# Kernel optimization log

Hardware: AMD Instinct MI355X
Metric: run time of the kernel (lower is better)

## Reference

```python
import jax, jax.numpy as jnp
import numpy as np

N, E, NF, EF = 50000, 1600000, 16, 8
H, HEADS, HD, L = 128, 4, 32, 3
EPS = 1e-5
NEG_SLOPE = 0.2


def layer_norm(x, g, b):
    mu = jnp.mean(x, axis=-1, keepdims=True)
    var = jnp.mean((x - mu) ** 2, axis=-1, keepdims=True)
    return g * (x - mu) * jax.lax.rsqrt(var + EPS) + b


def setup_inputs() -> dict:
    key = jax.random.key(0)
    ks = jax.random.split(key, 16)
    s = 0.02
    return {
        "x": jax.random.normal(ks[0], (N, NF), jnp.float32),
        "edge_index": jax.random.randint(ks[1], (2, E), 0, N, jnp.int32),
        "edge_attr": jax.random.normal(ks[2], (E, EF), jnp.float32),
        "Wn": jax.random.normal(ks[3], (NF, H), jnp.float32) * s,
        "bn": jnp.zeros((H,), jnp.float32),
        "We": jax.random.normal(ks[4], (EF, H), jnp.float32) * s,
        "be": jnp.zeros((H,), jnp.float32),
        "ln_g": jnp.ones((L, H), jnp.float32),
        "ln_b": jnp.zeros((L, H), jnp.float32),
        "Wg": jax.random.normal(ks[5], (L, H, HEADS * HD), jnp.float32) * s,
        "att_s": jax.random.normal(ks[6], (L, HEADS, HD), jnp.float32) * s,
        "att_d": jax.random.normal(ks[7], (L, HEADS, HD), jnp.float32) * s,
        "att_e": jax.random.normal(ks[8], (L, HEADS, HD), jnp.float32) * s,
        "W_edge": jax.random.normal(ks[9], (L, H, HEADS * HD), jnp.float32) * s,
        "bg": jnp.zeros((L, HEADS * HD), jnp.float32),
    }


def reference(x, edge_index, edge_attr, Wn, bn, We, be, ln_g, ln_b, Wg, att_s, att_d, att_e, W_edge, bg):
    n = x.shape[0]
    h = x @ Wn + bn                      # [N, H] node embedding
    e = edge_attr @ We + be              # [E, H] edge embedding
    src, dst = edge_index[0], edge_index[1]
    # PyG add_self_loops(fill_value='mean'): self-loop attr = mean of incoming edge attrs
    cnt = jax.ops.segment_sum(jnp.ones((e.shape[0],), e.dtype), dst, num_segments=n)
    loop_attr = jax.ops.segment_sum(e, dst, num_segments=n) / jnp.maximum(cnt, 1.0)[:, None]
    ar = jnp.arange(n, dtype=src.dtype)
    src_f = jnp.concatenate([src, ar])   # [E+N]
    dst_f = jnp.concatenate([dst, ar])
    e_f = jnp.concatenate([e, loop_attr], axis=0)  # [E+N, H]
    for i in range(Wg.shape[0]):
        x_in = layer_norm(h, ln_g[i], ln_b[i])               # pre-norm
        xs = (x_in @ Wg[i]).reshape(n, HEADS, HD)            # [N, heads, hd]
        ep = (e_f @ W_edge[i]).reshape(-1, HEADS, HD)        # [E+N, heads, hd]
        a_src = jnp.sum(xs * att_s[i], axis=-1)              # [N, heads]
        a_dst = jnp.sum(xs * att_d[i], axis=-1)
        a_edge = jnp.sum(ep * att_e[i], axis=-1)             # [E+N, heads]
        alpha = jax.nn.leaky_relu(a_src[src_f] + a_dst[dst_f] + a_edge, NEG_SLOPE)
        # scatter-softmax over edges sharing a destination node
        alpha = alpha - jax.ops.segment_max(alpha, dst_f, num_segments=n)[dst_f]
        ex = jnp.exp(alpha)
        w = ex / jax.ops.segment_sum(ex, dst_f, num_segments=n)[dst_f]  # [E+N, heads]
        msg = w[:, :, None] * xs[src_f]                      # [E+N, heads, hd]
        out = jax.ops.segment_sum(msg, dst_f, num_segments=n).reshape(n, HEADS * HD) + bg[i]
        h = h + jax.nn.relu(out)                             # proj is Identity; dropout eval-mode
    graph_emb = jnp.mean(h, axis=0, keepdims=True)           # batch=None path
    return h, graph_emb
```

## Files before the change

### kernel.cpp

```cpp
#include <hip/hip_runtime.h>

#define NN 50000
#define EE 1600000
#define HC 128
#define EPSV 1e-5f
#define NEGS 0.2f

#define NB_H0 6250
#define NB_HIST 6250
#define NB_PREP 230

typedef __bf16 bf16x8 __attribute__((ext_vector_type(8)));
typedef __bf16 bf16x2 __attribute__((ext_vector_type(2)));
typedef float f32x4 __attribute__((ext_vector_type(4)));

static inline int cdiv(int a, int b) { return (a + b - 1) / b; }

__device__ inline float blo(unsigned v) { return __uint_as_float(v << 16); }
__device__ inline float bhi(unsigned v) { return __uint_as_float(v & 0xffff0000u); }
__device__ inline unsigned pkbf(float a, float b) {
  bf16x2 p;
  p.x = (__bf16)a;
  p.y = (__bf16)b;
  return *reinterpret_cast<unsigned*>(&p);
}

__device__ inline float dec_e4m3(unsigned u) {
  unsigned bits = ((u & 0x80u) << 24) | ((u & 0x7Fu) << 20);
  return __uint_as_float(bits) * 0x1p120f;
}
__device__ inline unsigned enc_e4m3(float v) {
  unsigned b = __float_as_uint(v * 0x1p-120f);
  unsigned mag = (b & 0x7fffffffu) + 0x00080000u;
  return ((b >> 24) & 0x80u) | ((mag >> 20) & 0x7Fu);
}
__device__ inline unsigned enc4_e4m3(const float* r) {
  return enc_e4m3(r[0]) | (enc_e4m3(r[1]) << 8) | (enc_e4m3(r[2]) << 16) | (enc_e4m3(r[3]) << 24);
}

__global__ __launch_bounds__(256) void k_pre(const float* __restrict__ x, const float* __restrict__ Wn,
                                             const float* __restrict__ bn, const float* __restrict__ lng,
                                             const float* __restrict__ lnb, float* __restrict__ h,
                                             __bf16* __restrict__ xln, const int* __restrict__ ei,
                                             int* __restrict__ cnt, const float* __restrict__ We,
                                             const float* __restrict__ be, const float* __restrict__ Wed,
                                             const float* __restrict__ atte, float* __restrict__ Pc,
                                             const float* __restrict__ Wg, const float* __restrict__ atts,
                                             const float* __restrict__ attd, __bf16* __restrict__ wgt,
                                             int nb_hist) {
  int b = blockIdx.x;
  int t = threadIdx.x;
  if (b < NB_H0) {
    int idx = b * 256 + t;
    int n = idx >> 5, c4 = (idx & 31) * 4;
    float4 acc = *(const float4*)(bn + c4);
    const float* xr = x + (size_t)n * 16;
#pragma unroll
    for (int f = 0; f < 16; ++f) {
      float xv = xr[f];
      float4 wv = *(const float4*)(Wn + (size_t)f * HC + c4);
      acc.x += xv * wv.x;
      acc.y += xv * wv.y;
      acc.z += xv * wv.z;
      acc.w += xv * wv.w;
    }
    *(float4*)(h + (size_t)n * HC + c4) = acc;
    float s = acc.x + acc.y + acc.z + acc.w;
    float sq = acc.x * acc.x + acc.y * acc.y + acc.z * acc.z + acc.w * acc.w;
#pragma unroll
    for (int m = 1; m < 32; m <<= 1) {
      s += __shfl_xor(s, m);
      sq += __shfl_xor(sq, m);
    }
    float mu = s * (1.f / 128.f);
    float var = sq * (1.f / 128.f) - mu * mu;
    float rs = rsqrtf(fmaxf(var, 0.f) + EPSV);
    float4 g = *(const float4*)(lng + c4);
    float4 bb = *(const float4*)(lnb + c4);
    uint2 o;
    o.x = pkbf((acc.x - mu) * rs * g.x + bb.x, (acc.y - mu) * rs * g.y + bb.y);
    o.y = pkbf((acc.z - mu) * rs * g.z + bb.z, (acc.w - mu) * rs * g.w + bb.w);
    *(uint2*)(xln + (size_t)n * HC + c4) = o;
  } else if (b < NB_H0 + nb_hist) {
    int e = (b - NB_H0) * 256 + t;
    if (e < EE) atomicAdd(&cnt[ei[EE + e]], 1);
  } else if (b == NB_H0 + nb_hist) {
    __shared__ float v[128][4];
    for (int i = 0; i < 3; ++i) {
      if (t < 128) {
#pragma unroll
        for (int hh = 0; hh < 4; ++hh) {
          float s = 0.f;
          for (int hd = 0; hd < 32; ++hd)
            s += Wed[((size_t)i * 128 + t) * 128 + hh * 32 + hd] * atte[i * 128 + hh * 32 + hd];
          v[t][hh] = s;
        }
      }
      __syncthreads();
      if (t < 32) {
        int f = t >> 2, hh = t & 3;
        float s = 0.f;
        for (int c2 = 0; c2 < 128; ++c2) s += We[f * 128 + c2] * v[c2][hh];
        Pc[i * 36 + f * 4 + hh] = s;
      }
      if (t < 4) {
        float s = 0.f;
        for (int c2 = 0; c2 < 128; ++c2) s += be[c2] * v[c2][t];
        Pc[i * 36 + 32 + t] = s;
      }
      __syncthreads();
    }
  } else {
    int idx = (b - NB_H0 - nb_hist - 1) * 256 + t;
    if (idx >= 3 * 144 * 136) return;
    int i = idx / (144 * 136);
    int rem = idx - i * (144 * 136);
    int n = rem / 136, kp = rem - n * 136;
    float v = 0.f;
    if (kp < 128) {
      if (n < 128) {
        v = Wg[(size_t)i * 16384 + kp * 128 + n];
      } else if (n < 136) {
        int hh = (n - 128) & 3;
        const float* av = ((n < 132) ? atts : attd) + i * 128 + hh * 32;
        const float* wr = Wg + (size_t)i * 16384 + kp * 128 + hh * 32;
        float s = 0.f;
#pragma unroll
        for (int j = 0; j < 32; ++j) s += wr[j] * av[j];
        v = s;
      }
    }
    wgt[idx] = (__bf16)v;
  }
}

__global__ __launch_bounds__(1024) void k_scan1(const int* __restrict__ cnt, int* __restrict__ tmp,
                                                int* __restrict__ bsum) {
  __shared__ int lds[1024];
  int t = threadIdx.x;
  int i = blockIdx.x * 1024 + t;
  int v = (i < NN) ? cnt[i] : 0;
  lds[t] = v;
  __syncthreads();
  for (int off = 1; off < 1024; off <<= 1) {
    int u = (t >= off) ? lds[t - off] : 0;
    __syncthreads();
    lds[t] += u;
    __syncthreads();
  }
  if (i < NN) tmp[i] = lds[t] - v;
  if (t == 1023) bsum[blockIdx.x] = lds[1023];
}

__global__ void k_scan2(int* bsum, int nb) {
  if (threadIdx.x == 0 && blockIdx.x == 0) {
    int run = 0;
    for (int b = 0; b < nb; ++b) { int q = bsum[b]; bsum[b] = run; run += q; }
  }
}

__global__ __launch_bounds__(1024) void k_scan3(const int* __restrict__ tmp, const int* __restrict__ bsum,
                                                int* __restrict__ row_ptr, int* __restrict__ wr_ptr) {
  int t = threadIdx.x;
  int i = blockIdx.x * 1024 + t;
  if (i < NN) {
    int v = tmp[i] + bsum[blockIdx.x];
    row_ptr[i] = v;
    wr_ptr[i] = v;
  }
  if (i == 0) row_ptr[NN] = EE;
}

__global__ __launch_bounds__(256) void k_build(const int* __restrict__ ei, const float* __restrict__ ea,
                                               const float* __restrict__ Pc, int* __restrict__ cntr,
                                               unsigned char* __restrict__ rec8, int cap) {
  __shared__ float P[108];
  if (threadIdx.x < 108) P[threadIdx.x] = Pc[threadIdx.x];
  __syncthreads();
  int e = blockIdx.x * 256 + threadIdx.x;
  if (e >= EE) return;
  int s = ei[e], d = ei[EE + e];
  const float* ar = ea + (size_t)e * 8;
  float4 q0 = *(const float4*)ar;
  float4 q1 = *(const float4*)(ar + 4);
  float a[8] = {q0.x, q0.y, q0.z, q0.w, q1.x, q1.y, q1.z, q1.w};
  float r[3][4];
#pragma unroll
  for (int i = 0; i < 3; ++i) {
    const float* p = P + i * 36;
#pragma unroll
    for (int hh = 0; hh < 4; ++hh) {
      float s2 = p[32 + hh];
#pragma unroll
      for (int f = 0; f < 8; ++f) s2 += a[f] * p[f * 4 + hh];
      r[i][hh] = s2;
    }
  }
  size_t idx;
  int pos = atomicAdd(&cntr[d], 1);
  if (cap == 0) {
    idx = (size_t)pos;
  } else {
    if (pos >= cap) return;
    idx = (size_t)d * cap + pos;
  }
  uint4 rr;
  rr.x = (unsigned)s;
  rr.y = enc4_e4m3(r[0]);
  rr.z = enc4_e4m3(r[1]);
  rr.w = enc4_e4m3(r[2]);
  *(uint4*)(rec8 + idx * 16) = rr;
}

__global__ __launch_bounds__(256) void k_node(const __bf16* __restrict__ xln, const __bf16* __restrict__ wgt,
                                              __bf16* __restrict__ xsb, float* __restrict__ asrc,
                                              float* __restrict__ adst) {
  __shared__ __bf16 sA[128][136];
  __shared__ __bf16 sB[144][136];
  int t = threadIdx.x;
  int n0 = blockIdx.x * 128;
  {
    char* bd = (char*)&sB[0][0];
    const char* bs = (const char*)wgt;
    for (int off = t * 16; off < 144 * 136 * 2; off += 4096)
      *(uint4*)(bd + off) = *(const uint4*)(bs + off);
  }
  {
    uint4 z = make_uint4(0, 0, 0, 0);
#pragma unroll
    for (int u = t; u < 128 * 16; u += 256) {
      int row = u >> 4, ck = (u & 15) * 8;
      int n = n0 + row;
      uint4 v = (n < NN) ? *(const uint4*)(xln + (size_t)n * HC + ck) : z;
      *(uint4*)&sA[row][ck] = v;
    }
  }
  __syncthreads();
  int lane = t & 63;
  int c15 = lane & 15, g = lane >> 4;
  int m0w = (t >> 6) * 32;
  f32x4 acc[18];
#pragma unroll
  for (int i = 0; i < 18; ++i) acc[i] = (f32x4){0.f, 0.f, 0.f, 0.f};
#pragma unroll
  for (int ks = 0; ks < 4; ++ks) {
    bf16x8 a0 = *(const bf16x8*)&sA[m0w + c15][ks * 32 + g * 8];
    bf16x8 a1 = *(const bf16x8*)&sA[m0w + 16 + c15][ks * 32 + g * 8];
#pragma unroll
    for (int nt = 0; nt < 9; ++nt) {
      bf16x8 bv = *(const bf16x8*)&sB[nt * 16 + c15][ks * 32 + g * 8];
      acc[nt] = __builtin_amdgcn_mfma_f32_16x16x32_bf16(a0, bv, acc[nt], 0, 0, 0);
      acc[9 + nt] = __builtin_amdgcn_mfma_f32_16x16x32_bf16(a1, bv, acc[9 + nt], 0, 0, 0);
    }
  }
#pragma unroll
  for (int mt = 0; mt < 2; ++mt) {
    int nbase = n0 + m0w + mt * 16 + g * 4;
#pragma unroll
    for (int r = 0; r < 4; ++r) {
      int n = nbase + r;
      if (n < NN) {
        __bf16* op = xsb + (size_t)n * HC + c15;
#pragma unroll
        for (int nt = 0; nt < 8; ++nt) op[nt * 16] = (__bf16)acc[mt * 9 + nt][r];
        float av = acc[mt * 9 + 8][r];
        if (c15 < 4) asrc[(size_t)n * 4 + c15] = av;
        else if (c15 < 8) adst[(size_t)n * 4 + c15 - 4] = av;
      }
    }
  }
}

__global__ __launch_bounds__(256) void k_aggr(const int* __restrict__ row_ptr, const int* __restrict__ deg,
                                              int cap, const unsigned char* __restrict__ rec8, int layer,
                                              const __bf16* __restrict__ xsb, const float* __restrict__ asrc,
                                              const float* __restrict__ adst, const float* __restrict__ bgi,
                                              float* __restrict__ h, const float* __restrict__ lng2,
                                              const float* __restrict__ lnb2, __bf16* __restrict__ xln) {
  int wid = (blockIdx.x * 256 + threadIdx.x) >> 6;
  if (wid >= NN) return;
  int lane = threadIdx.x & 63;
  int ch0 = 2 * lane, head = lane >> 4;
  int um = lane & 7;
  int sbase = head << 4;
  int aoff = 4 + 4 * layer + head;
  int j0, j1;
  if (cap == 0) {
    j0 = row_ptr[wid];
    j1 = row_ptr[wid + 1];
  } else {
    j0 = wid * cap;
    int dg = deg[wid];
    if (dg > cap) dg = cap;
    j1 = j0 + dg;
  }
  float ad = adst[(size_t)wid * 4 + head];
  float acc0 = 0.f, acc1 = 0.f, dsum = 0.f, aes = 0.f;
  int nfull = (j1 - j0) >> 3;
  int j = j0 + nfull * 8;
  if (nfull > 0) {
    int ss[8], ssn[8];
#pragma unroll
    for (int u = 0; u < 8; ++u) ss[u] = *(const int*)(rec8 + (size_t)(j0 + u) * 16);
    for (int c = 0; c < nfull; ++c) {
      int jc = j0 + c * 8;
      if (c + 1 < nfull) {
#pragma unroll
        for (int u = 0; u < 8; ++u) ssn[u] = *(const int*)(rec8 + (size_t)(jc + 8 + u) * 16);
      } else {
#pragma unroll
        for (int u = 0; u < 8; ++u) ssn[u] = ss[u];
      }
      float av = dec_e4m3(rec8[(size_t)(jc + um) * 16 + aoff]);
      float as = asrc[(size_t)ss[um] * 4 + head];
      unsigned xv[8];
#pragma unroll
      for (int u = 0; u < 8; ++u) xv[u] = *(const unsigned*)(xsb + (size_t)ss[u] * HC + ch0);
      float alpha = as + ad + av;
      alpha = alpha > 0.f ? alpha : NEGS * alpha;
      float em = __expf(alpha);
      aes += av;
#pragma unroll
      for (int u = 0; u < 8; ++u) {
        float e = __shfl(em, sbase + u);
        acc0 += e * blo(xv[u]);
        acc1 += e * bhi(xv[u]);
        dsum += e;
      }
#pragma unroll
      for (int u = 0; u < 8; ++u) ss[u] = ssn[u];
    }
  }
  aes += __shfl_xor(aes, 1);
  aes += __shfl_xor(aes, 2);
  aes += __shfl_xor(aes, 4);
  for (; j < j1; ++j) {
    int s0 = *(const int*)(rec8 + (size_t)j * 16);
    float v0 = dec_e4m3(rec8[(size_t)j * 16 + aoff]);
    float as0 = asrc[(size_t)s0 * 4 + head];
    unsigned x0 = *(const unsigned*)(xsb + (size_t)s0 * HC + ch0);
    float a0 = as0 + ad + v0;
    a0 = a0 > 0.f ? a0 : NEGS * a0;
    float e0 = __expf(a0);
    acc0 += e0 * blo(x0);
    acc1 += e0 * bhi(x0);
    dsum += e0;
    aes += v0;
  }
  int dg = j1 - j0;
  float aself = (dg > 0) ? aes / (float)dg : 0.f;
  float al = asrc[(size_t)wid * 4 + head] + ad + aself;
  al = al > 0.f ? al : NEGS * al;
  float exl = __expf(al);
  unsigned xv = *(const unsigned*)(xsb + (size_t)wid * HC + ch0);
  float inv = 1.f / (dsum + exl);
  float o0 = (acc0 + exl * blo(xv)) * inv;
  float o1 = (acc1 + exl * bhi(xv)) * inv;
  float* hp = h + (size_t)wid * HC;
  float n0v = hp[ch0] + fmaxf(0.f, o0 + bgi[ch0]);
  float n1v = hp[ch0 + 1] + fmaxf(0.f, o1 + bgi[ch0 + 1]);
  hp[ch0] = n0v;
  hp[ch0 + 1] = n1v;
  if (xln) {
    float s = n0v + n1v, sq = n0v * n0v + n1v * n1v;
#pragma unroll
    for (int m = 1; m < 64; m <<= 1) {
      s += __shfl_xor(s, m);
      sq += __shfl_xor(sq, m);
    }
    float mu = s * (1.f / 128.f);
    float var = sq * (1.f / 128.f) - mu * mu;
    float rs = rsqrtf(fmaxf(var, 0.f) + EPSV);
    unsigned p = pkbf((n0v - mu) * rs * lng2[ch0] + lnb2[ch0], (n1v - mu) * rs * lng2[ch0 + 1] + lnb2[ch0 + 1]);
    *(unsigned*)(xln + (size_t)wid * HC + ch0) = p;
  }
}

__global__ __launch_bounds__(256) void k_emb(const float* __restrict__ h, float* __restrict__ emb) {
  int t = blockIdx.x * 256 + threadIdx.x;
  int stride = gridDim.x * 256;
  float s = 0.f;
  for (int i = t; i < NN * HC; i += stride) s += h[i];
  __shared__ float red[256];
  red[threadIdx.x] = s;
  __syncthreads();
  if (threadIdx.x < 128) {
    float v2 = red[threadIdx.x] + red[threadIdx.x + 128];
    atomicAdd(&emb[threadIdx.x], v2 * (1.f / NN));
  }
}

extern "C" void kernel_launch(void* const* d_in, const int* in_sizes, int n_in, void* d_out, int out_size,
                              void* d_ws, size_t ws_size, hipStream_t stream) {
  (void)in_sizes; (void)n_in; (void)out_size;
  const float* x = (const float*)d_in[0];
  const int* ei = (const int*)d_in[1];
  const float* ea = (const float*)d_in[2];
  const float* Wn = (const float*)d_in[3];
  const float* bn = (const float*)d_in[4];
  const float* We = (const float*)d_in[5];
  const float* be = (const float*)d_in[6];
  const float* lng = (const float*)d_in[7];
  const float* lnb = (const float*)d_in[8];
  const float* Wg = (const float*)d_in[9];
  const float* atts = (const float*)d_in[10];
  const float* attd = (const float*)d_in[11];
  const float* atte = (const float*)d_in[12];
  const float* Wed = (const float*)d_in[13];
  const float* bg = (const float*)d_in[14];
  float* h = (float*)d_out;
  float* emb = h + (size_t)NN * HC;

  char* w = (char*)d_ws;
  size_t off = 0;
  auto alloc = [&](size_t bytes) {
    void* p = w + off;
    off = (off + bytes + 255) & ~(size_t)255;
    return p;
  };
  __bf16* xsb = (__bf16*)alloc((size_t)NN * HC * 2);
  __bf16* xln = (__bf16*)alloc((size_t)NN * HC * 2);
  float* asrc = (float*)alloc((size_t)NN * 4 * 4);
  float* adst = (float*)alloc((size_t)NN * 4 * 4);
  int* cnt = (int*)alloc((size_t)NN * 4);
  int* row_ptr = (int*)alloc((size_t)(NN + 1) * 4);
  int* wr_ptr = (int*)alloc((size_t)NN * 4);
  int* bsum = (int*)alloc(256);
  int* stmp = (int*)alloc((size_t)NN * 4);
  float* Pc = (float*)alloc(3 * 36 * 4);
  __bf16* wgt = (__bf16*)alloc((size_t)3 * 144 * 136 * 2);

  size_t avail = (ws_size > off + 4096) ? (ws_size - off - 4096) : 0;
  size_t capv = avail / ((size_t)NN * 16);
  int cap = 0;
  if (capv >= 72) cap = (capv > 96) ? 96 : (int)capv;
  unsigned char* rec8 = (unsigned char*)alloc(cap ? (size_t)NN * cap * 16 : (size_t)EE * 16);

  hipMemsetAsync(cnt, 0, (size_t)NN * 4, stream);
  hipMemsetAsync(emb, 0, HC * 4, stream);

  if (cap) {
    k_pre<<<NB_H0 + 1 + NB_PREP, 256, 0, stream>>>(x, Wn, bn, lng, lnb, h, xln, ei, cnt, We, be, Wed, atte,
                                                   Pc, Wg, atts, attd, wgt, 0);
    k_build<<<cdiv(EE, 256), 256, 0, stream>>>(ei, ea, Pc, cnt, rec8, cap);
  } else {
    k_pre<<<NB_H0 + NB_HIST + 1 + NB_PREP, 256, 0, stream>>>(x, Wn, bn, lng, lnb, h, xln, ei, cnt, We, be,
                                                             Wed, atte, Pc, Wg, atts, attd, wgt, NB_HIST);
    int nb = cdiv(NN, 1024);
    k_scan1<<<nb, 1024, 0, stream>>>(cnt, stmp, bsum);
    k_scan2<<<1, 64, 0, stream>>>(bsum, nb);
    k_scan3<<<nb, 1024, 0, stream>>>(stmp, bsum, row_ptr, wr_ptr);
    k_build<<<cdiv(EE, 256), 256, 0, stream>>>(ei, ea, Pc, wr_ptr, rec8, 0);
  }

  for (int i = 0; i < 3; ++i) {
    k_node<<<cdiv(NN, 128), 256, 0, stream>>>(xln, wgt + (size_t)i * 144 * 136, xsb, asrc, adst);
    const float* g2 = (i < 2) ? (lng + (i + 1) * HC) : nullptr;
    const float* b2 = (i < 2) ? (lnb + (i + 1) * HC) : nullptr;
    __bf16* xo = (i < 2) ? xln : nullptr;
    k_aggr<<<cdiv(NN, 4), 256, 0, stream>>>(row_ptr, cnt, cap, rec8, i, xsb, asrc, adst, bg + i * HC, h,
                                            g2, b2, xo);
  }
  k_emb<<<512, 256, 0, stream>>>(h, emb);
}
```

Baseline: 420.7 us.

## Store node features as fp8 e4m3 and fuse layer-0 node GEMM into build

Changes the projected node feature buffer xs from bf16 to fp8 e4m3, which halves the bytes gathered per edge in the aggregation kernel at the cost of extra decode ALU work and lower precision. The layer-0 node GEMM is also merged into the edge-build launch as extra blocks, so it overlaps with the atomic-heavy build and one launch is saved. In the fallback path build and node are launched separately.

```diff
diff --git a/kernel.cpp b/kernel.cpp
--- a/kernel.cpp
+++ b/kernel.cpp
@@ -9,6 +9,8 @@
 #define NB_H0 6250
 #define NB_HIST 6250
 #define NB_PREP 230
+#define NB_BUILD 6250
+#define NB_NODE 391
 
 typedef __bf16 bf16x8 __attribute__((ext_vector_type(8)));
 typedef __bf16 bf16x2 __attribute__((ext_vector_type(2)));
@@ -171,13 +173,12 @@
   if (i == 0) row_ptr[NN] = EE;
 }
 
-__global__ __launch_bounds__(256) void k_build(const int* __restrict__ ei, const float* __restrict__ ea,
-                                               const float* __restrict__ Pc, int* __restrict__ cntr,
-                                               unsigned char* __restrict__ rec8, int cap) {
-  __shared__ float P[108];
-  if (threadIdx.x < 108) P[threadIdx.x] = Pc[threadIdx.x];
+__device__ inline void build_body(int bb, int t, const int* __restrict__ ei, const float* __restrict__ ea,
+                                  const float* __restrict__ Pc, int* __restrict__ cntr,
+                                  unsigned char* __restrict__ rec8, int cap, float* P) {
+  if (t < 108) P[t] = Pc[t];
   __syncthreads();
-  int e = blockIdx.x * 256 + threadIdx.x;
+  int e = bb * 256 + t;
   if (e >= EE) return;
   int s = ei[e], d = ei[EE + e];
   const float* ar = ea + (size_t)e * 8;
@@ -212,13 +213,10 @@
   *(uint4*)(rec8 + idx * 16) = rr;
 }
 
-__global__ __launch_bounds__(256) void k_node(const __bf16* __restrict__ xln, const __bf16* __restrict__ wgt,
-                                              __bf16* __restrict__ xsb, float* __restrict__ asrc,
-                                              float* __restrict__ adst) {
-  __shared__ __bf16 sA[128][136];
-  __shared__ __bf16 sB[144][136];
-  int t = threadIdx.x;
-  int n0 = blockIdx.x * 128;
+__device__ inline void node_body(int nb, int t, const __bf16* __restrict__ xln, const __bf16* __restrict__ wgt,
+                                 unsigned char* __restrict__ xsb, float* __restrict__ asrc,
+                                 float* __restrict__ adst, __bf16 (*sA)[136], __bf16 (*sB)[136]) {
+  int n0 = nb * 128;
   {
     char* bd = (char*)&sB[0][0];
     const char* bs = (const char*)wgt;
@@ -260,9 +258,9 @@
     for (int r = 0; r < 4; ++r) {
       int n = nbase + r;
       if (n < NN) {
-        __bf16* op = xsb + (size_t)n * HC + c15;
-#pragma unroll
-        for (int nt = 0; nt < 8; ++nt) op[nt * 16] = (__bf16)acc[mt * 9 + nt][r];
+        unsigned char* op = xsb + (size_t)n * HC + c15;
+#pragma unroll
+        for (int nt = 0; nt < 8; ++nt) op[nt * 16] = (unsigned char)enc_e4m3(acc[mt * 9 + nt][r]);
         float av = acc[mt * 9 + 8][r];
         if (c15 < 4) asrc[(size_t)n * 4 + c15] = av;
         else if (c15 < 8) adst[(size_t)n * 4 + c15 - 4] = av;
@@ -271,12 +269,38 @@
   }
 }
 
+__global__ __launch_bounds__(256) void k_bn(const int* __restrict__ ei, const float* __restrict__ ea,
+                                            const float* __restrict__ Pc, int* __restrict__ cntr,
+                                            unsigned char* __restrict__ rec8, int cap,
+                                            const __bf16* __restrict__ xln, const __bf16* __restrict__ wgt,
+                                            unsigned char* __restrict__ xsb, float* __restrict__ asrc,
+                                            float* __restrict__ adst, int nbuild) {
+  __shared__ __bf16 sA[128][136];
+  __shared__ __bf16 sB[144][136];
+  int b = blockIdx.x;
+  int t = threadIdx.x;
+  if (b < nbuild) {
+    build_body(b, t, ei, ea, Pc, cntr, rec8, cap, (float*)&sA[0][0]);
+  } else {
+    node_body(b - nbuild, t, xln, wgt, xsb, asrc, adst, sA, sB);
+  }
+}
+
+__global__ __launch_bounds__(256) void k_node(const __bf16* __restrict__ xln, const __bf16* __restrict__ wgt,
+                                              unsigned char* __restrict__ xsb, float* __restrict__ asrc,
+                                              float* __restrict__ adst) {
+  __shared__ __bf16 sA[128][136];
+  __shared__ __bf16 sB[144][136];
+  node_body(blockIdx.x, threadIdx.x, xln, wgt, xsb, asrc, adst, sA, sB);
+}
+
 __global__ __launch_bounds__(256) void k_aggr(const int* __restrict__ row_ptr, const int* __restrict__ deg,
                                               int cap, const unsigned char* __restrict__ rec8, int layer,
-                                              const __bf16* __restrict__ xsb, const float* __restrict__ asrc,
-                                              const float* __restrict__ adst, const float* __restrict__ bgi,
-                                              float* __restrict__ h, const float* __restrict__ lng2,
-                                              const float* __restrict__ lnb2, __bf16* __restrict__ xln) {
+                                              const unsigned char* __restrict__ xsb,
+                                              const float* __restrict__ asrc, const float* __restrict__ adst,
+                                              const float* __restrict__ bgi, float* __restrict__ h,
+                                              const float* __restrict__ lng2, const float* __restrict__ lnb2,
+                                              __bf16* __restrict__ xln) {
   int wid = (blockIdx.x * 256 + threadIdx.x) >> 6;
   if (wid >= NN) return;
   int lane = threadIdx.x & 63;
@@ -313,9 +337,10 @@
       }
       float av = dec_e4m3(rec8[(size_t)(jc + um) * 16 + aoff]);
       float as = asrc[(size_t)ss[um] * 4 + head];
-      unsigned xv[8];
-#pragma unroll
-      for (int u = 0; u < 8; ++u) xv[u] = *(const unsigned*)(xsb + (size_t)ss[u] * HC + ch0);
+      unsigned short xv[8];
+#pragma unroll
+      for (int u = 0; u < 8; ++u)
+        xv[u] = *(const unsigned short*)(xsb + (size_t)ss[u] * HC + ch0);
       float alpha = as + ad + av;
       alpha = alpha > 0.f ? alpha : NEGS * alpha;
       float em = __expf(alpha);
@@ -323,8 +348,8 @@
 #pragma unroll
       for (int u = 0; u < 8; ++u) {
         float e = __shfl(em, sbase + u);
-        acc0 += e * blo(xv[u]);
-        acc1 += e * bhi(xv[u]);
+        acc0 += e * dec_e4m3(xv[u] & 0xFFu);
+        acc1 += e * dec_e4m3((unsigned)xv[u] >> 8);
         dsum += e;
       }
 #pragma unroll
@@ -338,12 +363,12 @@
     int s0 = *(const int*)(rec8 + (size_t)j * 16);
     float v0 = dec_e4m3(rec8[(size_t)j * 16 + aoff]);
     float as0 = asrc[(size_t)s0 * 4 + head];
-    unsigned x0 = *(const unsigned*)(xsb + (size_t)s0 * HC + ch0);
+    unsigned short x0 = *(const unsigned short*)(xsb + (size_t)s0 * HC + ch0);
     float a0 = as0 + ad + v0;
     a0 = a0 > 0.f ? a0 : NEGS * a0;
     float e0 = __expf(a0);
-    acc0 += e0 * blo(x0);
-    acc1 += e0 * bhi(x0);
+    acc0 += e0 * dec_e4m3(x0 & 0xFFu);
+    acc1 += e0 * dec_e4m3((unsigned)x0 >> 8);
     dsum += e0;
     aes += v0;
   }
@@ -352,10 +377,10 @@
   float al = asrc[(size_t)wid * 4 + head] + ad + aself;
   al = al > 0.f ? al : NEGS * al;
   float exl = __expf(al);
-  unsigned xv = *(const unsigned*)(xsb + (size_t)wid * HC + ch0);
+  unsigned short xw = *(const unsigned short*)(xsb + (size_t)wid * HC + ch0);
   float inv = 1.f / (dsum + exl);
-  float o0 = (acc0 + exl * blo(xv)) * inv;
-  float o1 = (acc1 + exl * bhi(xv)) * inv;
+  float o0 = (acc0 + exl * dec_e4m3(xw & 0xFFu)) * inv;
+  float o1 = (acc1 + exl * dec_e4m3((unsigned)xw >> 8)) * inv;
   float* hp = h + (size_t)wid * HC;
   float n0v = hp[ch0] + fmaxf(0.f, o0 + bgi[ch0]);
   float n1v = hp[ch0 + 1] + fmaxf(0.f, o1 + bgi[ch0 + 1]);
@@ -418,7 +443,7 @@
     off = (off + bytes + 255) & ~(size_t)255;
     return p;
   };
-  __bf16* xsb = (__bf16*)alloc((size_t)NN * HC * 2);
+  unsigned char* xsb = (unsigned char*)alloc((size_t)NN * HC);
   __bf16* xln = (__bf16*)alloc((size_t)NN * HC * 2);
   float* asrc = (float*)alloc((size_t)NN * 4 * 4);
   float* adst = (float*)alloc((size_t)NN * 4 * 4);
@@ -442,7 +467,8 @@
   if (cap) {
     k_pre<<<NB_H0 + 1 + NB_PREP, 256, 0, stream>>>(x, Wn, bn, lng, lnb, h, xln, ei, cnt, We, be, Wed, atte,
                                                    Pc, Wg, atts, attd, wgt, 0);
-    k_build<<<cdiv(EE, 256), 256, 0, stream>>>(ei, ea, Pc, cnt, rec8, cap);
+    k_bn<<<NB_BUILD + NB_NODE, 256, 0, stream>>>(ei, ea, Pc, cnt, rec8, cap, xln, wgt, xsb, asrc, adst,
+                                                 NB_BUILD);
   } else {
     k_pre<<<NB_H0 + NB_HIST + 1 + NB_PREP, 256, 0, stream>>>(x, Wn, bn, lng, lnb, h, xln, ei, cnt, We, be,
                                                              Wed, atte, Pc, Wg, atts, attd, wgt, NB_HIST);
@@ -450,11 +476,13 @@
     k_scan1<<<nb, 1024, 0, stream>>>(cnt, stmp, bsum);
     k_scan2<<<1, 64, 0, stream>>>(bsum, nb);
     k_scan3<<<nb, 1024, 0, stream>>>(stmp, bsum, row_ptr, wr_ptr);
-    k_build<<<cdiv(EE, 256), 256, 0, stream>>>(ei, ea, Pc, wr_ptr, rec8, 0);
+    k_bn<<<cdiv(EE, 256), 256, 0, stream>>>(ei, ea, Pc, wr_ptr, rec8, 0, xln, wgt, xsb, asrc, adst,
+                                            cdiv(EE, 256));
+    k_node<<<NB_NODE, 256, 0, stream>>>(xln, wgt, xsb, asrc, adst);
   }
 
   for (int i = 0; i < 3; ++i) {
-    k_node<<<cdiv(NN, 128), 256, 0, stream>>>(xln, wgt + (size_t)i * 144 * 136, xsb, asrc, adst);
+    if (i > 0) k_node<<<NB_NODE, 256, 0, stream>>>(xln, wgt + (size_t)i * 144 * 136, xsb, asrc, adst);
     const float* g2 = (i < 2) ? (lng + (i + 1) * HC) : nullptr;
     const float* b2 = (i < 2) ? (lnb + (i + 1) * HC) : nullptr;
     __bf16* xo = (i < 2) ? xln : nullptr;
```

New measurement: 441.1 us. +4.8%, slower.

## Merge edge build with node init into one kernel; nontemporal edge record loads

Applied to the files above, without the earlier changes.

Moves the tiny edge-coefficient reduction into its own single-block kernel, then fuses the edge-record build, the initial node embedding and layer-norm, and the weight prep into one launch on the capped-bucket path. This drops a kernel boundary and lets the build blocks overlap with the node work. Edge record reads in the aggregation loop now use nontemporal loads so the streamed records do not evict reused node features from cache. The cost is an extra tiny serial kernel that runs ahead of the fused launch.

```diff
diff --git a/kernel.cpp b/kernel.cpp
--- a/kernel.cpp
+++ b/kernel.cpp
@@ -9,6 +9,8 @@
 #define NB_H0 6250
 #define NB_HIST 6250
 #define NB_PREP 230
+#define NB_BUILD 6250
+#define NB_NODE 391
 
 typedef __bf16 bf16x8 __attribute__((ext_vector_type(8)));
 typedef __bf16 bf16x2 __attribute__((ext_vector_type(2)));
@@ -38,100 +40,177 @@
   return enc_e4m3(r[0]) | (enc_e4m3(r[1]) << 8) | (enc_e4m3(r[2]) << 16) | (enc_e4m3(r[3]) << 24);
 }
 
-__global__ __launch_bounds__(256) void k_pre(const float* __restrict__ x, const float* __restrict__ Wn,
-                                             const float* __restrict__ bn, const float* __restrict__ lng,
-                                             const float* __restrict__ lnb, float* __restrict__ h,
-                                             __bf16* __restrict__ xln, const int* __restrict__ ei,
-                                             int* __restrict__ cnt, const float* __restrict__ We,
-                                             const float* __restrict__ be, const float* __restrict__ Wed,
-                                             const float* __restrict__ atte, float* __restrict__ Pc,
-                                             const float* __restrict__ Wg, const float* __restrict__ atts,
-                                             const float* __restrict__ attd, __bf16* __restrict__ wgt,
-                                             int nb_hist) {
-  int b = blockIdx.x;
+__global__ __launch_bounds__(128) void k_wcoef(const float* __restrict__ We, const float* __restrict__ be,
+                                               const float* __restrict__ Wed, const float* __restrict__ atte,
+                                               float* __restrict__ Pc) {
+  __shared__ float v[128][4];
   int t = threadIdx.x;
+  for (int i = 0; i < 3; ++i) {
+#pragma unroll
+    for (int hh = 0; hh < 4; ++hh) {
+      float s = 0.f;
+      for (int hd = 0; hd < 32; ++hd)
+        s += Wed[((size_t)i * 128 + t) * 128 + hh * 32 + hd] * atte[i * 128 + hh * 32 + hd];
+      v[t][hh] = s;
+    }
+    __syncthreads();
+    if (t < 32) {
+      int f = t >> 2, hh = t & 3;
+      float s = 0.f;
+      for (int c2 = 0; c2 < 128; ++c2) s += We[f * 128 + c2] * v[c2][hh];
+      Pc[i * 36 + f * 4 + hh] = s;
+    }
+    if (t < 4) {
+      float s = 0.f;
+      for (int c2 = 0; c2 < 128; ++c2) s += be[c2] * v[c2][t];
+      Pc[i * 36 + 32 + t] = s;
+    }
+    __syncthreads();
+  }
+}
+
+
+__device__ inline void h0_body(int idx, const float* __restrict__ x, const float* __restrict__ Wn,
+                               const float* __restrict__ bn, const float* __restrict__ lng,
+                               const float* __restrict__ lnb, float* __restrict__ h,
+                               __bf16* __restrict__ xln) {
+  int n = idx >> 5, c4 = (idx & 31) * 4;
+  float4 acc = *(const float4*)(bn + c4);
+  const float* xr = x + (size_t)n * 16;
+#pragma unroll
+  for (int f = 0; f < 16; ++f) {
+    float xv = xr[f];
+    float4 wv = *(const float4*)(Wn + (size_t)f * HC + c4);
+    acc.x += xv * wv.x;
+    acc.y += xv * wv.y;
+    acc.z += xv * wv.z;
+    acc.w += xv * wv.w;
+  }
+  *(float4*)(h + (size_t)n * HC + c4) = acc;
+  float s = acc.x + acc.y + acc.z + acc.w;
+  float sq = acc.x * acc.x + acc.y * acc.y + acc.z * acc.z + acc.w * acc.w;
+#pragma unroll
+  for (int m = 1; m < 32; m <<= 1) {
+    s += __shfl_xor(s, m);
+    sq += __shfl_xor(sq, m);
+  }
+  float mu = s * (1.f / 128.f);
+  float var = sq * (1.f / 128.f) - mu * mu;
+  float rs = rsqrtf(fmaxf(var, 0.f) + EPSV);
+  float4 g = *(const float4*)(lng + c4);
+  float4 bb = *(const float4*)(lnb + c4);
+  uint2 o;
+  o.x = pkbf((acc.x - mu) * rs * g.x + bb.x, (acc.y - mu) * rs * g.y + bb.y);
+  o.y = pkbf((acc.z - mu) * rs * g.z + bb.z, (acc.w - mu) * rs * g.w + bb.w);
+  *(uint2*)(xln + (size_t)n * HC + c4) = o;
+}
+
+__device__ inline void prep_body(int idx, const float* __restrict__ Wg, const float* __restrict__ atts,
+                                 const float* __restrict__ attd, __bf16* __restrict__ wgt) {
+  if (idx >= 3 * 144 * 136) return;
+  int i = idx / (144 * 136);
+  int rem = idx - i * (144 * 136);
+  int n = rem / 136, kp = rem - n * 136;
+  float v = 0.f;
+  if (kp < 128) {
+    if (n < 128) {
+      v = Wg[(size_t)i * 16384 + kp * 128 + n];
+    } else if (n < 136) {
+      int hh = (n - 128) & 3;
+      const float* av = ((n < 132) ? atts : attd) + i * 128 + hh * 32;
+      const float* wr = Wg + (size_t)i * 16384 + kp * 128 + hh * 32;
+      float s = 0.f;
+#pragma unroll
+      for (int j = 0; j < 32; ++j) s += wr[j] * av[j];
+      v = s;
+    }
+  }
+  wgt[idx] = (__bf16)v;
+}
+
+__device__ inline void build_body(int bb, int t, const int* __restrict__ ei, const float* __restrict__ ea,
+                                  const float* __restrict__ Pc, int* __restrict__ cntr,
+                                  unsigned char* __restrict__ rec8, int cap, float* P) {
+  if (t < 108) P[t] = Pc[t];
+  __syncthreads();
+  int e = bb * 256 + t;
+  if (e >= EE) return;
+  int s = ei[e], d = ei[EE + e];
+  const float* ar = ea + (size_t)e * 8;
+  float4 q0 = *(const float4*)ar;
+  float4 q1 = *(const float4*)(ar + 4);
+  float a[8] = {q0.x, q0.y, q0.z, q0.w, q1.x, q1.y, q1.z, q1.w};
+  float r[3][4];
+#pragma unroll
+  for (int i = 0; i < 3; ++i) {
+    const float* p = P + i * 36;
+#pragma unroll
+    for (int hh = 0; hh < 4; ++hh) {
+      float s2 = p[32 + hh];
+#pragma unroll
+      for (int f = 0; f < 8; ++f) s2 += a[f] * p[f * 4 + hh];
+      r[i][hh] = s2;
+    }
+  }
+  size_t idx;
+  int pos = atomicAdd(&cntr[d], 1);
+  if (cap == 0) {
+    idx = (size_t)pos;
+  } else {
+    if (pos >= cap) return;
+    idx = (size_t)d * cap + pos;
+  }
+  uint4 rr;
+  rr.x = (unsigned)s;
+  rr.y = enc4_e4m3(r[0]);
+  rr.z = enc4_e4m3(r[1]);
+  rr.w = enc4_e4m3(r[2]);
+  *(uint4*)(rec8 + idx * 16) = rr;
+}
+
+__global__ __launch_bounds__(256) void k_mega(const int* __restrict__ ei, const float* __restrict__ ea,
+                                              const float* __restrict__ Pc, int* __restrict__ cnt,
+                                              unsigned char* __restrict__ rec8, int cap,
+                                              const float* __restrict__ x, const float* __restrict__ Wn,
+                                              const float* __restrict__ bn, const float* __restrict__ lng,
+                                              const float* __restrict__ lnb, float* __restrict__ h,
+                                              __bf16* __restrict__ xln, const float* __restrict__ Wg,
+                                              const float* __restrict__ atts, const float* __restrict__ attd,
+                                              __bf16* __restrict__ wgt) {
+  __shared__ float P[108];
+  int b = blockIdx.x, t = threadIdx.x;
+  if (b < NB_BUILD) {
+    build_body(b, t, ei, ea, Pc, cnt, rec8, cap, P);
+  } else if (b < NB_BUILD + NB_H0) {
+    h0_body((b - NB_BUILD) * 256 + t, x, Wn, bn, lng, lnb, h, xln);
+  } else {
+    prep_body((b - NB_BUILD - NB_H0) * 256 + t, Wg, atts, attd, wgt);
+  }
+}
+
+__global__ __launch_bounds__(256) void k_fb(const float* __restrict__ x, const float* __restrict__ Wn,
+                                            const float* __restrict__ bn, const float* __restrict__ lng,
+                                            const float* __restrict__ lnb, float* __restrict__ h,
+                                            __bf16* __restrict__ xln, const int* __restrict__ ei,
+                                            int* __restrict__ cnt, const float* __restrict__ Wg,
+                                            const float* __restrict__ atts, const float* __restrict__ attd,
+                                            __bf16* __restrict__ wgt) {
+  int b = blockIdx.x, t = threadIdx.x;
   if (b < NB_H0) {
-    int idx = b * 256 + t;
-    int n = idx >> 5, c4 = (idx & 31) * 4;
-    float4 acc = *(const float4*)(bn + c4);
-    const float* xr = x + (size_t)n * 16;
-#pragma unroll
-    for (int f = 0; f < 16; ++f) {
-      float xv = xr[f];
-      float4 wv = *(const float4*)(Wn + (size_t)f * HC + c4);
-      acc.x += xv * wv.x;
-      acc.y += xv * wv.y;
-      acc.z += xv * wv.z;
-      acc.w += xv * wv.w;
-    }
-    *(float4*)(h + (size_t)n * HC + c4) = acc;
-    float s = acc.x + acc.y + acc.z + acc.w;
-    float sq = acc.x * acc.x + acc.y * acc.y + acc.z * acc.z + acc.w * acc.w;
-#pragma unroll
-    for (int m = 1; m < 32; m <<= 1) {
-      s += __shfl_xor(s, m);
-      sq += __shfl_xor(sq, m);
-    }
-    float mu = s * (1.f / 128.f);
-    float var = sq * (1.f / 128.f) - mu * mu;
-    float rs = rsqrtf(fmaxf(var, 0.f) + EPSV);
-    float4 g = *(const float4*)(lng + c4);
-    float4 bb = *(const float4*)(lnb + c4);
-    uint2 o;
-    o.x = pkbf((acc.x - mu) * rs * g.x + bb.x, (acc.y - mu) * rs * g.y + bb.y);
-    o.y = pkbf((acc.z - mu) * rs * g.z + bb.z, (acc.w - mu) * rs * g.w + bb.w);
-    *(uint2*)(xln + (size_t)n * HC + c4) = o;
-  } else if (b < NB_H0 + nb_hist) {
+    h0_body(b * 256 + t, x, Wn, bn, lng, lnb, h, xln);
+  } else if (b < NB_H0 + NB_HIST) {
     int e = (b - NB_H0) * 256 + t;
     if (e < EE) atomicAdd(&cnt[ei[EE + e]], 1);
-  } else if (b == NB_H0 + nb_hist) {
-    __shared__ float v[128][4];
-    for (int i = 0; i < 3; ++i) {
-      if (t < 128) {
-#pragma unroll
-        for (int hh = 0; hh < 4; ++hh) {
-          float s = 0.f;
-          for (int hd = 0; hd < 32; ++hd)
-            s += Wed[((size_t)i * 128 + t) * 128 + hh * 32 + hd] * atte[i * 128 + hh * 32 + hd];
-          v[t][hh] = s;
-        }
-      }
-      __syncthreads();
-      if (t < 32) {
-        int f = t >> 2, hh = t & 3;
-        float s = 0.f;
-        for (int c2 = 0; c2 < 128; ++c2) s += We[f * 128 + c2] * v[c2][hh];
-        Pc[i * 36 + f * 4 + hh] = s;
-      }
-      if (t < 4) {
-        float s = 0.f;
-        for (int c2 = 0; c2 < 128; ++c2) s += be[c2] * v[c2][t];
-        Pc[i * 36 + 32 + t] = s;
-      }
-      __syncthreads();
-    }
   } else {
-    int idx = (b - NB_H0 - nb_hist - 1) * 256 + t;
-    if (idx >= 3 * 144 * 136) return;
-    int i = idx / (144 * 136);
-    int rem = idx - i * (144 * 136);
-    int n = rem / 136, kp = rem - n * 136;
-    float v = 0.f;
-    if (kp < 128) {
-      if (n < 128) {
-        v = Wg[(size_t)i * 16384 + kp * 128 + n];
-      } else if (n < 136) {
-        int hh = (n - 128) & 3;
-        const float* av = ((n < 132) ? atts : attd) + i * 128 + hh * 32;
-        const float* wr = Wg + (size_t)i * 16384 + kp * 128 + hh * 32;
-        float s = 0.f;
-#pragma unroll
-        for (int j = 0; j < 32; ++j) s += wr[j] * av[j];
-        v = s;
-      }
-    }
-    wgt[idx] = (__bf16)v;
-  }
+    prep_body((b - NB_H0 - NB_HIST) * 256 + t, Wg, atts, attd, wgt);
+  }
+}
+
+__global__ __launch_bounds__(256) void k_build(const int* __restrict__ ei, const float* __restrict__ ea,
+                                               const float* __restrict__ Pc, int* __restrict__ cntr,
+                                               unsigned char* __restrict__ rec8, int cap) {
+  __shared__ float P[108];
+  build_body(blockIdx.x, threadIdx.x, ei, ea, Pc, cntr, rec8, cap, P);
 }
 
 __global__ __launch_bounds__(1024) void k_scan1(const int* __restrict__ cnt, int* __restrict__ tmp,
@@ -169,47 +248,6 @@
     wr_ptr[i] = v;
   }
   if (i == 0) row_ptr[NN] = EE;
-}
-
-__global__ __launch_bounds__(256) void k_build(const int* __restrict__ ei, const float* __restrict__ ea,
-                                               const float* __restrict__ Pc, int* __restrict__ cntr,
-                                               unsigned char* __restrict__ rec8, int cap) {
-  __shared__ float P[108];
-  if (threadIdx.x < 108) P[threadIdx.x] = Pc[threadIdx.x];
-  __syncthreads();
-  int e = blockIdx.x * 256 + threadIdx.x;
-  if (e >= EE) return;
-  int s = ei[e], d = ei[EE + e];
-  const float* ar = ea + (size_t)e * 8;
-  float4 q0 = *(const float4*)ar;
-  float4 q1 = *(const float4*)(ar + 4);
-  float a[8] = {q0.x, q0.y, q0.z, q0.w, q1.x, q1.y, q1.z, q1.w};
-  float r[3][4];
-#pragma unroll
-  for (int i = 0; i < 3; ++i) {
-    const float* p = P + i * 36;
-#pragma unroll
-    for (int hh = 0; hh < 4; ++hh) {
-      float s2 = p[32 + hh];
-#pragma unroll
-      for (int f = 0; f < 8; ++f) s2 += a[f] * p[f * 4 + hh];
-      r[i][hh] = s2;
-    }
-  }
-  size_t idx;
-  int pos = atomicAdd(&cntr[d], 1);
-  if (cap == 0) {
-    idx = (size_t)pos;
-  } else {
-    if (pos >= cap) return;
-    idx = (size_t)d * cap + pos;
-  }
-  uint4 rr;
-  rr.x = (unsigned)s;
-  rr.y = enc4_e4m3(r[0]);
-  rr.z = enc4_e4m3(r[1]);
-  rr.w = enc4_e4m3(r[2]);
-  *(uint4*)(rec8 + idx * 16) = rr;
 }
 
 __global__ __launch_bounds__(256) void k_node(const __bf16* __restrict__ xln, const __bf16* __restrict__ wgt,
@@ -301,17 +339,19 @@
   if (nfull > 0) {
     int ss[8], ssn[8];
 #pragma unroll
-    for (int u = 0; u < 8; ++u) ss[u] = *(const int*)(rec8 + (size_t)(j0 + u) * 16);
+    for (int u = 0; u < 8; ++u)
+      ss[u] = __builtin_nontemporal_load((const int*)(rec8 + (size_t)(j0 + u) * 16));
     for (int c = 0; c < nfull; ++c) {
       int jc = j0 + c * 8;
       if (c + 1 < nfull) {
 #pragma unroll
-        for (int u = 0; u < 8; ++u) ssn[u] = *(const int*)(rec8 + (size_t)(jc + 8 + u) * 16);
+        for (int u = 0; u < 8; ++u)
+          ssn[u] = __builtin_nontemporal_load((const int*)(rec8 + (size_t)(jc + 8 + u) * 16));
       } else {
 #pragma unroll
         for (int u = 0; u < 8; ++u) ssn[u] = ss[u];
       }
-      float av = dec_e4m3(rec8[(size_t)(jc + um) * 16 + aoff]);
+      float av = dec_e4m3(__builtin_nontemporal_load(rec8 + (size_t)(jc + um) * 16 + aoff));
       float as = asrc[(size_t)ss[um] * 4 + head];
       unsigned xv[8];
 #pragma unroll
@@ -439,13 +479,14 @@
   hipMemsetAsync(cnt, 0, (size_t)NN * 4, stream);
   hipMemsetAsync(emb, 0, HC * 4, stream);
 
+  k_wcoef<<<1, 128, 0, stream>>>(We, be, Wed, atte, Pc);
+
   if (cap) {
-    k_pre<<<NB_H0 + 1 + NB_PREP, 256, 0, stream>>>(x, Wn, bn, lng, lnb, h, xln, ei, cnt, We, be, Wed, atte,
-                                                   Pc, Wg, atts, attd, wgt, 0);
-    k_build<<<cdiv(EE, 256), 256, 0, stream>>>(ei, ea, Pc, cnt, rec8, cap);
+    k_mega<<<NB_BUILD + NB_H0 + NB_PREP, 256, 0, stream>>>(ei, ea, Pc, cnt, rec8, cap, x, Wn, bn, lng, lnb,
+                                                           h, xln, Wg, atts, attd, wgt);
   } else {
-    k_pre<<<NB_H0 + NB_HIST + 1 + NB_PREP, 256, 0, stream>>>(x, Wn, bn, lng, lnb, h, xln, ei, cnt, We, be,
-                                                             Wed, atte, Pc, Wg, atts, attd, wgt, NB_HIST);
+    k_fb<<<NB_H0 + NB_HIST + NB_PREP, 256, 0, stream>>>(x, Wn, bn, lng, lnb, h, xln, ei, cnt, Wg, atts,
+                                                        attd, wgt);
     int nb = cdiv(NN, 1024);
     k_scan1<<<nb, 1024, 0, stream>>>(cnt, stmp, bsum);
     k_scan2<<<1, 64, 0, stream>>>(bsum, nb);
@@ -454,7 +495,7 @@
   }
 
   for (int i = 0; i < 3; ++i) {
-    k_node<<<cdiv(NN, 128), 256, 0, stream>>>(xln, wgt + (size_t)i * 144 * 136, xsb, asrc, adst);
+    k_node<<<NB_NODE, 256, 0, stream>>>(xln, wgt + (size_t)i * 144 * 136, xsb, asrc, adst);
     const float* g2 = (i < 2) ? (lng + (i + 1) * HC) : nullptr;
     const float* b2 = (i < 2) ? (lnb + (i + 1) * HC) : nullptr;
     __bf16* xo = (i < 2) ? xln : nullptr;
```

After: 447.3 us. 1.06x slower.
